# Kernel tuning notes

Hardware: AMD Instinct MI355X
Metric: run time of the kernel (lower is better)

The kernel has to match this reference:

```python
import jax, jax.numpy as jnp
import numpy as np

B = 2048          # number of graphs in the batch
ACT_DIM = 14      # nodes per graph (act_dim)
C = 128           # in_channels
H = 256           # hidden_size


def _pair_edges(n):
    ii, jj = np.meshgrid(np.arange(n), np.arange(n), indexing='ij')
    m = ii != jj
    return np.stack([ii[m], jj[m]], axis=1)  # [n*(n-1), 2]


def setup_inputs() -> dict:
    key = jax.random.key(0)
    ks = jax.random.split(key, 12)
    edges_np = _pair_edges(ACT_DIM)                       # [182, 2]
    offs = (np.arange(B) * ACT_DIM)[:, None, None]
    batched = (edges_np[None] + offs).reshape(-1, 2)      # [B*182, 2]
    edge_index = jnp.asarray(batched.T, dtype=jnp.int64 if jax.config.jax_enable_x64 else jnp.int32)
    edges = jnp.asarray(edges_np, dtype=jnp.int32)

    def lin(k, o, i):
        return jax.random.normal(k, (o, i), jnp.float32) * (1.0 / np.sqrt(i))

    return {
        'state': jax.random.normal(ks[0], (B * ACT_DIM, C), jnp.float32),
        'conv_w': lin(ks[1], C, C),
        'conv_b': jnp.zeros((C,), jnp.float32),
        'lin1_w': lin(ks[2], H, 2 * C),
        'lin1_b': jax.random.normal(ks[3], (H,), jnp.float32) * 0.01,
        'lin2_w': lin(ks[4], H, H),
        'lin2_b': jax.random.normal(ks[5], (H,), jnp.float32) * 0.01,
        'mu_w': lin(ks[6], 1, H),
        'mu_b': jnp.zeros((1,), jnp.float32),
        'sig_w': lin(ks[7], 1, H),
        'sig_b': jnp.zeros((1,), jnp.float32),
        'noise': jax.random.normal(ks[8], (B, edges_np.shape[0]), jnp.float32),
        'edge_index': edge_index,
        'edges': edges,
    }


def _gcn_conv(x, edge_index, w, b):
    # Standard GCNConv: add self-loops, symmetric normalization, x @ W^T, scatter-add, + bias.
    n = x.shape[0]
    loops = jnp.arange(n, dtype=edge_index.dtype)
    src = jnp.concatenate([edge_index[0], loops])
    dst = jnp.concatenate([edge_index[1], loops])
    deg = jax.ops.segment_sum(jnp.ones_like(src, dtype=x.dtype), dst, num_segments=n)
    dinv = jax.lax.rsqrt(deg)  # deg >= 1 because of self-loops
    norm = dinv[src] * dinv[dst]                       # [E+N]
    xw = x @ w.T                                       # [N, C]
    msg = xw[src] * norm[:, None]                      # gather + scale
    return jax.ops.segment_sum(msg, dst, num_segments=n) + b


def reference(state, conv_w, conv_b, lin1_w, lin1_b, lin2_w, lin2_b,
              mu_w, mu_b, sig_w, sig_b, noise, edge_index, edges):
    out = jax.nn.relu(_gcn_conv(state, edge_index, conv_w, conv_b))
    x = (out + state).reshape(-1, ACT_DIM, C)          # [B, 14, C]
    es, ed = edges[:, 0], edges[:, 1]
    ef = jnp.concatenate([x[:, es, :], x[:, ed, :]], axis=2)   # [B, E, 2C]
    h = jax.nn.leaky_relu(jnp.einsum('bec,hc->beh', ef, lin1_w) + lin1_b)
    h = jax.nn.leaky_relu(jnp.einsum('beh,gh->beg', h, lin2_w) + lin2_b)
    mu = jax.nn.softplus(jnp.einsum('beh,oh->beo', h, mu_w) + mu_b)[..., 0]   # [B, E]
    std = jax.nn.softplus(jnp.einsum('beh,oh->beo', h, sig_w) + sig_b)[..., 0]
    action = mu + std * noise                          # Normal rsample with fixed eps
    log_prob = jnp.sum(
        -0.5 * ((action - mu) / std) ** 2 - jnp.log(std) - 0.5 * jnp.log(2.0 * jnp.pi),
        axis=-1)                                       # [B]
    return action, log_prob
```

## Files before the change

kernel.cpp:

```cpp
#include <hip/hip_runtime.h>
#include <hip/hip_bf16.h>

#define ACT 14
#define CC 128
#define HH 256
#define EPB 182
#define NB 2048
#define M2 (NB*EPB)
#define NS 520
#define LP_CONST (-182.0f * 0.91893853320467274f)

typedef short s16x8 __attribute__((ext_vector_type(8)));
typedef float f32x4 __attribute__((ext_vector_type(4)));
typedef int   i32x4 __attribute__((ext_vector_type(4)));
typedef float f32x16 __attribute__((ext_vector_type(16)));

__device__ __forceinline__ short f2bf(float f) {
    unsigned u = __float_as_uint(f);
    unsigned r = (u + 0x7fffu + ((u >> 16) & 1u)) >> 16;
    return (short)r;
}
__device__ __forceinline__ float b2f(short s) {
    return __uint_as_float(((unsigned)(unsigned short)s) << 16);
}
__device__ __forceinline__ float bflo(int m) { return __uint_as_float(((unsigned)m) << 16); }
__device__ __forceinline__ float bfhi(int m) { return __uint_as_float((unsigned)m & 0xffff0000u); }
__device__ __forceinline__ float leaky(float x) { return fmaxf(x, 0.01f * x); }
__device__ __forceinline__ float softplusf(float x) { return x > 15.f ? x : log1pf(expf(x)); }

union bf2u { __hip_bfloat162 h; int i; };
__device__ __forceinline__ int pk_bf16(float a, float b) {
    bf2u u; u.h = __float22bfloat162_rn(make_float2(a, b));
    return u.i;
}

__global__ __launch_bounds__(256) void prep_kernel(
    const float* __restrict__ conv_w, const float* __restrict__ lin1_w,
    const float* __restrict__ lin2_w, const float* __restrict__ mu_w,
    const float* __restrict__ sig_w,
    short* __restrict__ W2bf, short* __restrict__ W1bf,
    short* __restrict__ cwTbf, short* __restrict__ w1sTbf,
    int* __restrict__ msbf)
{
    int i = blockIdx.x * 256 + threadIdx.x;
    W2bf[i] = f2bf(lin2_w[i]);
    {
        int n = i >> 7, k = i & 127;
        float v = (n < 256) ? lin1_w[n * 256 + k] : lin1_w[(n - 256) * 256 + 128 + k];
        W1bf[i] = f2bf(v);
    }
    if (i < 16384) {
        int k = i >> 7, j = i & 127;
        cwTbf[i] = f2bf(conv_w[j * 128 + k]);
    }
    if (i < 32768) {
        int k = i >> 8, h = i & 255;
        w1sTbf[i] = f2bf(lin1_w[h * 256 + k] + lin1_w[h * 256 + 128 + k]);
    }
    if (i < 256) msbf[i] = pk_bf16(mu_w[i], sig_w[i]);
}

__global__ __launch_bounds__(512, 4) void actor_kernel(
    const float* __restrict__ state, const short* __restrict__ W1bf,
    const short* __restrict__ W2bf,
    const short* __restrict__ cwTbf, const float* __restrict__ conv_b,
    const short* __restrict__ w1sTbf, const float* __restrict__ lin1_b,
    const float* __restrict__ lin2_b, const int* __restrict__ msbf,
    const float* __restrict__ mu_b, const float* __restrict__ sig_b,
    const float* __restrict__ noise, const int* __restrict__ edges,
    float* __restrict__ out)
{
    __shared__ short h1L[2][8192];
    __shared__ short nodeL[2 * ACT * NS];
    __shared__ float ssumL[2][128];
    __shared__ float gL[2][128];
    __shared__ float wL[2][256];
    __shared__ float b2L[256];
    __shared__ int   msL[256];
    __shared__ float mu_acc[384], sg_acc[384];
    __shared__ float lp_acc[2];

    short* stateL = &h1L[0][0];
    float* pp     = (float*)&h1L[0][5120];

    const int t = threadIdx.x, b = blockIdx.x;
    const int lane = t & 63, ln = lane & 15, q = lane >> 4;
    const int w = t >> 6;
    const int l32 = lane & 31, hf = lane >> 5;

    #pragma unroll
    for (int it = 0; it < 2; ++it) {
        int idx = it * 512 + t;
        int bt = idx >> 9, row = (idx >> 5) & 15, c4 = idx & 31;
        int kk = c4 >> 3, k8 = (c4 & 7) * 4;
        int* dst = (int*)&stateL[bt * 2560 + kk * 640 + row * 40 + k8];
        if (row < ACT) {
            f32x4 x = *(const f32x4*)(state + ((size_t)(2 * b + bt) * ACT + row) * CC + c4 * 4);
            dst[0] = pk_bf16(x[0], x[1]); dst[1] = pk_bf16(x[2], x[3]);
        } else { dst[0] = 0; dst[1] = 0; }
    }
    if (t < 256) {
        b2L[t] = lin2_b[t];
        msL[t] = msbf[t];
    } else {
        int i = t - 256, bt = i >> 7, c = i & 127;
        const float* sp = state + (size_t)(2 * b + bt) * ACT * CC + c;
        float s = 0.f;
        #pragma unroll
        for (int r = 0; r < ACT; ++r) s += sp[r * CC];
        ssumL[bt][c] = s * (1.f / 14.f);
    }
    if (t < 384) { mu_acc[t] = 0.f; sg_acc[t] = 0.f; }
    if (t < 2) lp_acc[t] = 0.f;
    __syncthreads();

    {
        int bt = t >> 8, s = (t >> 7) & 1, j = t & 127;
        const float* ss = ssumL[bt];
        float a0 = 0.f, a1 = 0.f;
        #pragma unroll 4
        for (int kk = 0; kk < 64; kk += 2) {
            int k = s * 64 + kk;
            a0 += b2f(cwTbf[k * 128 + j]) * ss[k];
            a1 += b2f(cwTbf[(k + 1) * 128 + j]) * ss[k + 1];
        }
        pp[t] = a0 + a1;
    }
    __syncthreads();
    if (t < 256) {
        int bt = t >> 7, j = t & 127;
        float a = pp[bt * 256 + j] + pp[bt * 256 + 128 + j] + conv_b[j];
        gL[bt][j] = fmaxf(a, 0.f);
    }
    __syncthreads();
    {
        int bt = t >> 8, h = t & 255;
        const float* gg = gL[bt];
        float a0 = 0.f, a1 = 0.f, a2 = 0.f, a3 = 0.f;
        #pragma unroll 2
        for (int k = 0; k < 128; k += 4) {
            a0 += b2f(w1sTbf[k * 256 + h]) * gg[k];
            a1 += b2f(w1sTbf[(k + 1) * 256 + h]) * gg[k + 1];
            a2 += b2f(w1sTbf[(k + 2) * 256 + h]) * gg[k + 2];
            a3 += b2f(w1sTbf[(k + 3) * 256 + h]) * gg[k + 3];
        }
        wL[bt][h] = (a0 + a1) + (a2 + a3) + lin1_b[h];
    }
    __syncthreads();

    f32x4 zero4 = {0.f, 0.f, 0.f, 0.f};
    f32x4 nacc[2][4];
    #pragma unroll
    for (int bt = 0; bt < 2; ++bt) {
        nacc[bt][0] = zero4; nacc[bt][1] = zero4;
        nacc[bt][2] = zero4; nacc[bt][3] = zero4;
    }
    #pragma unroll
    for (int c = 0; c < 4; ++c) {
        s16x8 a80 = *(const s16x8*)&stateL[0 * 2560 + c * 640 + ln * 40 + q * 8];
        s16x8 a81 = *(const s16x8*)&stateL[1 * 2560 + c * 640 + ln * 40 + q * 8];
        #pragma unroll
        for (int i = 0; i < 4; ++i) {
            int ct = w + 8 * i;
            s16x8 b8 = *(const s16x8*)&W1bf[(size_t)(ct * 16 + ln) * CC + c * 32 + q * 8];
            nacc[0][i] = __builtin_amdgcn_mfma_f32_16x16x32_bf16(a80, b8, nacc[0][i], 0, 0, 0);
            nacc[1][i] = __builtin_amdgcn_mfma_f32_16x16x32_bf16(a81, b8, nacc[1][i], 0, 0, 0);
        }
    }
    #pragma unroll
    for (int bt = 0; bt < 2; ++bt)
        #pragma unroll
        for (int i = 0; i < 4; ++i) {
            int col = (w + 8 * i) * 16 + ln;
            float wadd = (col < HH) ? wL[bt][col] : 0.f;
            #pragma unroll
            for (int rg = 0; rg < 4; ++rg) {
                int node = q * 4 + rg;
                if (node < ACT) nodeL[(bt * ACT + node) * NS + col] = f2bf(nacc[bt][i][rg] + wadd);
            }
        }

    s16x8 wa[16];
    #pragma unroll
    for (int c = 0; c < 16; ++c)
        wa[c] = *(const s16x8*)&W2bf[(size_t)(w * 32 + l32) * HH + c * 16 + hf * 8];
    __syncthreads();

    auto build = [&](int tile, int bufi) {
        int bt = (tile >= 6) ? 1 : 0;
        int e32 = t & 31;
        int e = (tile - bt * 6) * 32 + e32;
        bool ok = e < EPB;
        int base = bt * ACT * NS;
        int uo = base, vo = base + HH;
        if (ok) { int2 p = ((const int2*)edges)[e]; uo += p.x * NS; vo += p.y * NS; }
        int sl = t >> 5;
        #pragma unroll
        for (int s = 0; s < 2; ++s) {
            int slot = sl + 16 * s;
            int chunk = slot >> 1, half = slot & 1;
            int koff = chunk * 16 + half * 8;
            int o[4] = {0, 0, 0, 0};
            if (ok) {
                s16x8 u8 = *(const s16x8*)&nodeL[uo + koff];
                s16x8 v8 = *(const s16x8*)&nodeL[vo + koff];
                const int* ui = (const int*)&u8;
                const int* vi = (const int*)&v8;
                #pragma unroll
                for (int j = 0; j < 4; ++j) {
                    int uu = ui[j], vv = vi[j];
                    float s0 = bflo(uu) + bflo(vv);
                    float s1 = bfhi(uu) + bfhi(vv);
                    o[j] = pk_bf16(leaky(s0), leaky(s1));
                }
            }
            *(s16x8*)&h1L[bufi][chunk * 512 + (half * 32 + e32) * 8] = *(const s16x8*)o;
        }
    };

    build(0, 0);
    for (int tile = 0; tile < 12; ++tile) {
        __syncthreads();
        if (tile < 11) build(tile + 1, (tile + 1) & 1);
        const int buf = tile & 1;
        f32x16 acc;
        #pragma unroll
        for (int r = 0; r < 16; ++r) acc[r] = 0.f;
        #pragma unroll
        for (int c = 0; c < 16; ++c) {
            s16x8 b8 = *(const s16x8*)&h1L[buf][c * 512 + lane * 8];
            acc = __builtin_amdgcn_mfma_f32_32x32x16_bf16(wa[c], b8, acc, 0, 0, 0);
        }
        int bt = (tile >= 6) ? 1 : 0;
        int col0 = (tile - bt * 6) * 32;
        float pmu = 0.f, psg = 0.f;
        const int nsb = w * 32 + 4 * hf;
        #pragma unroll
        for (int g = 0; g < 4; ++g) {
            f32x4 b4 = *(const f32x4*)&b2L[nsb + 8 * g];
            i32x4 m4 = *(const i32x4*)&msL[nsb + 8 * g];
            #pragma unroll
            for (int i = 0; i < 4; ++i) {
                float h2 = leaky(acc[g * 4 + i] + b4[i]);
                pmu += bflo(m4[i]) * h2;
                psg += bfhi(m4[i]) * h2;
            }
        }
        pmu += __shfl_xor(pmu, 32);
        psg += __shfl_xor(psg, 32);
        if (lane < 32) {
            atomicAdd(&mu_acc[bt * 192 + col0 + l32], pmu);
            atomicAdd(&sg_acc[bt * 192 + col0 + l32], psg);
        }
    }
    __syncthreads();

    float lpv = 0.f;
    {
        int bt = t >> 8, i = t & 255;
        if (i < EPB) {
            float mu = softplusf(mu_acc[bt * 192 + i] + mu_b[0]);
            float sd = softplusf(sg_acc[bt * 192 + i] + sig_b[0]);
            float z = noise[(size_t)(2 * b + bt) * EPB + i];
            out[(size_t)(2 * b + bt) * EPB + i] = mu + sd * z;
            lpv = -0.5f * z * z - logf(sd);
        }
    }
    #pragma unroll
    for (int off = 1; off < 64; off <<= 1) lpv += __shfl_xor(lpv, off);
    if (lane == 0) atomicAdd(&lp_acc[t >> 8], lpv);
    __syncthreads();
    if (t < 2) out[M2 + 2 * b + t] = lp_acc[t] + LP_CONST;
}

extern "C" void kernel_launch(void* const* d_in, const int* in_sizes, int n_in,
                              void* d_out, int out_size, void* d_ws, size_t ws_size,
                              hipStream_t stream)
{
    const float* state  = (const float*)d_in[0];
    const float* conv_w = (const float*)d_in[1];
    const float* conv_b = (const float*)d_in[2];
    const float* lin1_w = (const float*)d_in[3];
    const float* lin1_b = (const float*)d_in[4];
    const float* lin2_w = (const float*)d_in[5];
    const float* lin2_b = (const float*)d_in[6];
    const float* mu_w   = (const float*)d_in[7];
    const float* mu_b   = (const float*)d_in[8];
    const float* sig_w  = (const float*)d_in[9];
    const float* sig_b  = (const float*)d_in[10];
    const float* noise  = (const float*)d_in[11];
    const int*   edges  = (const int*)d_in[13];
    float* out = (float*)d_out;

    char* ws = (char*)d_ws;
    short* W2bf   = (short*)ws;  ws += 65536 * 2;
    short* W1bf   = (short*)ws;  ws += 65536 * 2;
    short* cwTbf  = (short*)ws;  ws += 16384 * 2;
    short* w1sTbf = (short*)ws;  ws += 32768 * 2;
    int*   msbf   = (int*)ws;    ws += 256 * 4;

    prep_kernel<<<256, 256, 0, stream>>>(conv_w, lin1_w, lin2_w, mu_w, sig_w,
                                         W2bf, W1bf, cwTbf, w1sTbf, msbf);
    actor_kernel<<<NB / 2, 512, 0, stream>>>(state, W1bf, W2bf,
                                             cwTbf, conv_b, w1sTbf, lin1_b,
                                             lin2_b, msbf, mu_b, sig_b,
                                             noise, edges, out);
}
```

Measured before the change: 209.6 us.

## Single-buffer edge tile LDS and vectorize conv/lin1 mean GEMVs

```diff
diff --git a/kernel.cpp b/kernel.cpp
--- a/kernel.cpp
+++ b/kernel.cpp
@@ -37,10 +37,10 @@
 __global__ __launch_bounds__(256) void prep_kernel(
     const float* __restrict__ conv_w, const float* __restrict__ lin1_w,
     const float* __restrict__ lin2_w, const float* __restrict__ mu_w,
-    const float* __restrict__ sig_w,
+    const float* __restrict__ sig_w, const float* __restrict__ lin2_b,
     short* __restrict__ W2bf, short* __restrict__ W1bf,
-    short* __restrict__ cwTbf, short* __restrict__ w1sTbf,
-    int* __restrict__ msbf)
+    short* __restrict__ cwbf, short* __restrict__ w1sbf,
+    int* __restrict__ msbf, int* __restrict__ b2p)
 {
     int i = blockIdx.x * 256 + threadIdx.x;
     W2bf[i] = f2bf(lin2_w[i]);
@@ -49,39 +49,36 @@
         float v = (n < 256) ? lin1_w[n * 256 + k] : lin1_w[(n - 256) * 256 + 128 + k];
         W1bf[i] = f2bf(v);
     }
-    if (i < 16384) {
-        int k = i >> 7, j = i & 127;
-        cwTbf[i] = f2bf(conv_w[j * 128 + k]);
-    }
+    if (i < 16384) cwbf[i] = f2bf(conv_w[i]);
     if (i < 32768) {
-        int k = i >> 8, h = i & 255;
-        w1sTbf[i] = f2bf(lin1_w[h * 256 + k] + lin1_w[h * 256 + 128 + k]);
+        int h = i >> 7, k = i & 127;
+        w1sbf[i] = f2bf(lin1_w[h * 256 + k] + lin1_w[h * 256 + 128 + k]);
     }
     if (i < 256) msbf[i] = pk_bf16(mu_w[i], sig_w[i]);
+    if (i < 128) b2p[i] = pk_bf16(lin2_b[2 * i], lin2_b[2 * i + 1]);
 }
 
 __global__ __launch_bounds__(512, 4) void actor_kernel(
     const float* __restrict__ state, const short* __restrict__ W1bf,
     const short* __restrict__ W2bf,
-    const short* __restrict__ cwTbf, const float* __restrict__ conv_b,
-    const short* __restrict__ w1sTbf, const float* __restrict__ lin1_b,
-    const float* __restrict__ lin2_b, const int* __restrict__ msbf,
+    const short* __restrict__ cwbf, const float* __restrict__ conv_b,
+    const short* __restrict__ w1sbf, const float* __restrict__ lin1_b,
+    const int* __restrict__ b2p, const int* __restrict__ msbf,
     const float* __restrict__ mu_b, const float* __restrict__ sig_b,
     const float* __restrict__ noise, const int* __restrict__ edges,
     float* __restrict__ out)
 {
-    __shared__ short h1L[2][8192];
+    __shared__ short h1L[8192];
     __shared__ short nodeL[2 * ACT * NS];
-    __shared__ float ssumL[2][128];
-    __shared__ float gL[2][128];
     __shared__ float wL[2][256];
-    __shared__ float b2L[256];
+    __shared__ int   b2pL[128];
     __shared__ int   msL[256];
     __shared__ float mu_acc[384], sg_acc[384];
     __shared__ float lp_acc[2];
 
-    short* stateL = &h1L[0][0];
-    float* pp     = (float*)&h1L[0][5120];
+    short* stateL = &h1L[0];
+    float* ssumLp = (float*)&h1L[5120];
+    float* gLp    = (float*)&h1L[5632];
 
     const int t = threadIdx.x, b = blockIdx.x;
     const int lane = t & 63, ln = lane & 15, q = lane >> 4;
@@ -100,51 +97,54 @@
         } else { dst[0] = 0; dst[1] = 0; }
     }
     if (t < 256) {
-        b2L[t] = lin2_b[t];
         msL[t] = msbf[t];
+        if (t < 128) b2pL[t] = b2p[t];
     } else {
         int i = t - 256, bt = i >> 7, c = i & 127;
         const float* sp = state + (size_t)(2 * b + bt) * ACT * CC + c;
         float s = 0.f;
         #pragma unroll
         for (int r = 0; r < ACT; ++r) s += sp[r * CC];
-        ssumL[bt][c] = s * (1.f / 14.f);
+        ssumLp[bt * 128 + c] = s * (1.f / 14.f);
     }
     if (t < 384) { mu_acc[t] = 0.f; sg_acc[t] = 0.f; }
     if (t < 2) lp_acc[t] = 0.f;
     __syncthreads();
 
-    {
-        int bt = t >> 8, s = (t >> 7) & 1, j = t & 127;
-        const float* ss = ssumL[bt];
-        float a0 = 0.f, a1 = 0.f;
-        #pragma unroll 4
-        for (int kk = 0; kk < 64; kk += 2) {
-            int k = s * 64 + kk;
-            a0 += b2f(cwTbf[k * 128 + j]) * ss[k];
-            a1 += b2f(cwTbf[(k + 1) * 128 + j]) * ss[k + 1];
-        }
-        pp[t] = a0 + a1;
-    }
-    __syncthreads();
     if (t < 256) {
         int bt = t >> 7, j = t & 127;
-        float a = pp[bt * 256 + j] + pp[bt * 256 + 128 + j] + conv_b[j];
-        gL[bt][j] = fmaxf(a, 0.f);
+        const short* cw = cwbf + j * CC;
+        const float* ss = ssumLp + bt * 128;
+        float a0 = 0.f, a1 = 0.f;
+        #pragma unroll
+        for (int c8 = 0; c8 < 16; ++c8) {
+            s16x8 w8 = *(const s16x8*)(cw + c8 * 8);
+            f32x4 s0 = *(const f32x4*)(ss + c8 * 8);
+            f32x4 s1 = *(const f32x4*)(ss + c8 * 8 + 4);
+            a0 += b2f(w8[0]) * s0[0]; a1 += b2f(w8[1]) * s0[1];
+            a0 += b2f(w8[2]) * s0[2]; a1 += b2f(w8[3]) * s0[3];
+            a0 += b2f(w8[4]) * s1[0]; a1 += b2f(w8[5]) * s1[1];
+            a0 += b2f(w8[6]) * s1[2]; a1 += b2f(w8[7]) * s1[3];
+        }
+        gLp[bt * 128 + j] = fmaxf(a0 + a1 + conv_b[j], 0.f);
     }
     __syncthreads();
     {
         int bt = t >> 8, h = t & 255;
-        const float* gg = gL[bt];
-        float a0 = 0.f, a1 = 0.f, a2 = 0.f, a3 = 0.f;
-        #pragma unroll 2
-        for (int k = 0; k < 128; k += 4) {
-            a0 += b2f(w1sTbf[k * 256 + h]) * gg[k];
-            a1 += b2f(w1sTbf[(k + 1) * 256 + h]) * gg[k + 1];
-            a2 += b2f(w1sTbf[(k + 2) * 256 + h]) * gg[k + 2];
-            a3 += b2f(w1sTbf[(k + 3) * 256 + h]) * gg[k + 3];
-        }
-        wL[bt][h] = (a0 + a1) + (a2 + a3) + lin1_b[h];
+        const short* ww = w1sbf + h * CC;
+        const float* gg = gLp + bt * 128;
+        float a0 = 0.f, a1 = 0.f;
+        #pragma unroll
+        for (int c8 = 0; c8 < 16; ++c8) {
+            s16x8 w8 = *(const s16x8*)(ww + c8 * 8);
+            f32x4 s0 = *(const f32x4*)(gg + c8 * 8);
+            f32x4 s1 = *(const f32x4*)(gg + c8 * 8 + 4);
+            a0 += b2f(w8[0]) * s0[0]; a1 += b2f(w8[1]) * s0[1];
+            a0 += b2f(w8[2]) * s0[2]; a1 += b2f(w8[3]) * s0[3];
+            a0 += b2f(w8[4]) * s1[0]; a1 += b2f(w8[5]) * s1[1];
+            a0 += b2f(w8[6]) * s1[2]; a1 += b2f(w8[7]) * s1[3];
+        }
+        wL[bt][h] = a0 + a1 + lin1_b[h];
     }
     __syncthreads();
 
@@ -186,7 +186,7 @@
         wa[c] = *(const s16x8*)&W2bf[(size_t)(w * 32 + l32) * HH + c * 16 + hf * 8];
     __syncthreads();
 
-    auto build = [&](int tile, int bufi) {
+    auto build = [&](int tile) {
         int bt = (tile >= 6) ? 1 : 0;
         int e32 = t & 31;
         int e = (tile - bt * 6) * 32 + e32;
@@ -214,21 +214,19 @@
                     o[j] = pk_bf16(leaky(s0), leaky(s1));
                 }
             }
-            *(s16x8*)&h1L[bufi][chunk * 512 + (half * 32 + e32) * 8] = *(const s16x8*)o;
+            *(s16x8*)&h1L[chunk * 512 + (half * 32 + e32) * 8] = *(const s16x8*)o;
         }
     };
 
-    build(0, 0);
     for (int tile = 0; tile < 12; ++tile) {
+        build(tile);
         __syncthreads();
-        if (tile < 11) build(tile + 1, (tile + 1) & 1);
-        const int buf = tile & 1;
         f32x16 acc;
         #pragma unroll
         for (int r = 0; r < 16; ++r) acc[r] = 0.f;
         #pragma unroll
         for (int c = 0; c < 16; ++c) {
-            s16x8 b8 = *(const s16x8*)&h1L[buf][c * 512 + lane * 8];
+            s16x8 b8 = *(const s16x8*)&h1L[c * 512 + lane * 8];
             acc = __builtin_amdgcn_mfma_f32_32x32x16_bf16(wa[c], b8, acc, 0, 0, 0);
         }
         int bt = (tile >= 6) ? 1 : 0;
@@ -237,14 +235,16 @@
         const int nsb = w * 32 + 4 * hf;
         #pragma unroll
         for (int g = 0; g < 4; ++g) {
-            f32x4 b4 = *(const f32x4*)&b2L[nsb + 8 * g];
+            int2 bp = *(const int2*)&b2pL[(nsb >> 1) + 4 * g];
             i32x4 m4 = *(const i32x4*)&msL[nsb + 8 * g];
-            #pragma unroll
-            for (int i = 0; i < 4; ++i) {
-                float h2 = leaky(acc[g * 4 + i] + b4[i]);
-                pmu += bflo(m4[i]) * h2;
-                psg += bfhi(m4[i]) * h2;
-            }
+            float b2v0 = bflo(bp.x), b2v1 = bfhi(bp.x);
+            float b2v2 = bflo(bp.y), b2v3 = bfhi(bp.y);
+            float h0 = leaky(acc[g * 4 + 0] + b2v0);
+            float h1 = leaky(acc[g * 4 + 1] + b2v1);
+            float h2 = leaky(acc[g * 4 + 2] + b2v2);
+            float h3 = leaky(acc[g * 4 + 3] + b2v3);
+            pmu += bflo(m4[0]) * h0 + bflo(m4[1]) * h1 + bflo(m4[2]) * h2 + bflo(m4[3]) * h3;
+            psg += bfhi(m4[0]) * h0 + bfhi(m4[1]) * h1 + bfhi(m4[2]) * h2 + bfhi(m4[3]) * h3;
         }
         pmu += __shfl_xor(pmu, 32);
         psg += __shfl_xor(psg, 32);
@@ -252,8 +252,8 @@
             atomicAdd(&mu_acc[bt * 192 + col0 + l32], pmu);
             atomicAdd(&sg_acc[bt * 192 + col0 + l32], psg);
         }
-    }
-    __syncthreads();
+        __syncthreads();
+    }
 
     float lpv = 0.f;
     {
@@ -293,16 +293,17 @@
     float* out = (float*)d_out;
 
     char* ws = (char*)d_ws;
-    short* W2bf   = (short*)ws;  ws += 65536 * 2;
-    short* W1bf   = (short*)ws;  ws += 65536 * 2;
-    short* cwTbf  = (short*)ws;  ws += 16384 * 2;
-    short* w1sTbf = (short*)ws;  ws += 32768 * 2;
-    int*   msbf   = (int*)ws;    ws += 256 * 4;
-
-    prep_kernel<<<256, 256, 0, stream>>>(conv_w, lin1_w, lin2_w, mu_w, sig_w,
-                                         W2bf, W1bf, cwTbf, w1sTbf, msbf);
+    short* W2bf  = (short*)ws;  ws += 65536 * 2;
+    short* W1bf  = (short*)ws;  ws += 65536 * 2;
+    short* cwbf  = (short*)ws;  ws += 16384 * 2;
+    short* w1sbf = (short*)ws;  ws += 32768 * 2;
+    int*   msbf  = (int*)ws;    ws += 256 * 4;
+    int*   b2p   = (int*)ws;    ws += 128 * 4;
+
+    prep_kernel<<<256, 256, 0, stream>>>(conv_w, lin1_w, lin2_w, mu_w, sig_w, lin2_b,
+                                         W2bf, W1bf, cwbf, w1sbf, msbf, b2p);
     actor_kernel<<<NB / 2, 512, 0, stream>>>(state, W1bf, W2bf,
-                                             cwTbf, conv_b, w1sTbf, lin1_b,
-                                             lin2_b, msbf, mu_b, sig_b,
+                                             cwbf, conv_b, w1sbf, lin1_b,
+                                             b2p, msbf, mu_b, sig_b,
                                              noise, edges, out);
 }
```

Result: slower. 218.2 us (+4.1%).
